# Optimization experiments

Hardware: AMD Instinct MI355X
Metric: run time of the kernel (lower is better)

Reference implementation:

```python
import jax, jax.numpy as jnp
import numpy as np


def setup_inputs() -> dict:
    key = jax.random.key(0)
    ks = jax.random.split(key, 7)
    b, t, c = 2, 2048, 1024
    s = 0.02  # keep pre-softmax logits in a sane range
    return {
        "query": jax.random.normal(ks[0], (b, t, c), jnp.float32),
        "key": jax.random.normal(ks[1], (b, t, c), jnp.float32),
        "value": jax.random.normal(ks[2], (b, t, c), jnp.float32),
        "in_proj_w": jax.random.normal(ks[3], (3 * c, c), jnp.float32) * s,
        "in_proj_b": jax.random.normal(ks[4], (3 * c,), jnp.float32) * s,
        "out_proj_w": jax.random.normal(ks[5], (c, c), jnp.float32) * s,
        "out_proj_b": jax.random.normal(ks[6], (c,), jnp.float32) * s,
        "window_size": 128,
    }


def reference(query, key, value, in_proj_w, in_proj_b, out_proj_w, out_proj_b, window_size):
    num_heads = 16
    b, t, c = query.shape
    hd = c // num_heads
    wq, wk, wv = in_proj_w[:c], in_proj_w[c:2 * c], in_proj_w[2 * c:]
    bq, bk, bv = in_proj_b[:c], in_proj_b[c:2 * c], in_proj_b[2 * c:]
    # project and split heads: [b, h, t, hd]
    q = (query @ wq.T + bq).reshape(b, t, num_heads, hd).transpose(0, 2, 1, 3)
    k = (key @ wk.T + bk).reshape(b, t, num_heads, hd).transpose(0, 2, 1, 3)
    v = (value @ wv.T + bv).reshape(b, t, num_heads, hd).transpose(0, 2, 1, 3)
    # NOTE: torch adds a *float* attn_mask to the logits. The original mask is
    # 1.0 inside the sliding window, 0.0 outside -- an additive +1 bias, NOT -inf.
    idx = jnp.arange(t)
    band = (jnp.abs(idx[:, None] - idx[None, :]) <= window_size).astype(q.dtype)  # [t, t]
    scale = 1.0 / jnp.sqrt(jnp.asarray(hd, q.dtype))
    logits = jnp.einsum("bhqd,bhkd->bhqk", q * scale, k) + band  # [b,h,t,t]
    attn = jax.nn.softmax(logits, axis=-1)
    out = jnp.einsum("bhqk,bhkd->bhqd", attn, v)  # [b,h,t,hd]
    out = out.transpose(0, 2, 1, 3).reshape(b, t, c)
    return out @ out_proj_w.T + out_proj_b
```

## Files before the change

### kernel.cpp

```cpp
#include <hip/hip_runtime.h>

typedef __attribute__((ext_vector_type(8)))  short short8;
typedef __attribute__((ext_vector_type(4)))  float f32x4;
typedef __attribute__((ext_vector_type(16))) float f32x16;

constexpr int B  = 2;
constexpr int T  = 2048;
constexpr int C  = 1024;
constexpr int H  = 16;
constexpr int HD = 64;

__device__ inline unsigned bf16rne(float a){
  unsigned u = __builtin_bit_cast(unsigned, a);
  u += 0x7fffu + ((u >> 16) & 1u);
  return u >> 16;
}
__device__ inline unsigned bf16pair(float a, float b){
  unsigned ua = __builtin_bit_cast(unsigned, a); ua += 0x7fffu + ((ua >> 16) & 1u);
  unsigned ub = __builtin_bit_cast(unsigned, b); ub += 0x7fffu + ((ub >> 16) & 1u);
  return (ua >> 16) | (ub & 0xffff0000u);
}
__device__ inline void gll16(const void* g, void* l){
  __builtin_amdgcn_global_load_lds(
      (const __attribute__((address_space(1))) unsigned*)g,
      (__attribute__((address_space(3))) unsigned*)l, 16, 0, 0);
}
__device__ inline float exp2f_(float x){
#if __has_builtin(__builtin_amdgcn_exp2f)
  return __builtin_amdgcn_exp2f(x);
#else
  return __builtin_exp2f(x);
#endif
}

__global__ void convert_k(const float* __restrict__ ipw, const float* __restrict__ opw,
                          const float* __restrict__ q, const float* __restrict__ k,
                          const float* __restrict__ v, unsigned* __restrict__ dst)
{
  const int i = blockIdx.x * 256 + threadIdx.x;
  const long e = (long)i * 4;
  const float* src; long off;
  if      (e <  3145728) { src = ipw; off = e; }
  else if (e <  4194304) { src = opw; off = e - 3145728; }
  else if (e <  8388608) { src = q;   off = e - 4194304; }
  else if (e < 12582912) { src = k;   off = e - 8388608; }
  else                   { src = v;   off = e - 12582912; }
  const float4 x = *(const float4*)(src + off);
  dst[i*2+0] = bf16pair(x.x, x.y);
  dst[i*2+1] = bf16pair(x.z, x.w);
}

template<int MODE>
__global__ __launch_bounds__(256, 2) void gemm_k(
    const unsigned short* __restrict__ A0, const unsigned short* __restrict__ A1,
    const unsigned short* __restrict__ A2,
    const unsigned short* __restrict__ Wb, const float* __restrict__ bias,
    unsigned short* __restrict__ Qb, unsigned short* __restrict__ Kb,
    unsigned short* __restrict__ Vt, float* __restrict__ outF)
{
  __shared__ __align__(16) char gsm[32768];
  unsigned short* As = (unsigned short*)gsm;
  unsigned short* Bs = (unsigned short*)(gsm + 16384);

  const int tid  = threadIdx.x, lane = tid & 63, wv = tid >> 6;
  const int wm   = wv & 1, wn = wv >> 1;
  const int bn   = blockIdx.x, bm = blockIdx.y;
  const int m16  = lane & 15, quad = lane >> 4;

  const int which = (MODE == 0) ? (bn >> 3) : 0;
  const unsigned short* A = (which == 0) ? A0 : (which == 1 ? A1 : A2);

  f32x4 acc[4][4];
#pragma unroll
  for (int i = 0; i < 4; i++)
#pragma unroll
    for (int j = 0; j < 4; j++) acc[i][j] = (f32x4){0.f, 0.f, 0.f, 0.f};

  const int srow = (lane >> 3);
  const int skp  = (lane & 7) * 8;

  for (int k0 = 0; k0 < 1024; k0 += 64) {
    __syncthreads();
#pragma unroll
    for (int p = 0; p < 4; p++) {
      const int row = wv*32 + p*8 + srow;
      gll16(A  + (size_t)(bm*128 + row)*1024 + k0 + skp, (char*)As + (wv*4+p)*1024);
      gll16(Wb + (size_t)(bn*128 + row)*1024 + k0 + skp, (char*)Bs + (wv*4+p)*1024);
    }
    __syncthreads();

    short8 af[2][4], bf2[2][4];
#pragma unroll
    for (int kh = 0; kh < 2; kh++) {
#pragma unroll
      for (int i = 0; i < 4; i++)
        af[kh][i] = *(const short8*)((const char*)As + (wm*64 + i*16 + m16)*128 + kh*64 + quad*16);
#pragma unroll
      for (int j = 0; j < 4; j++)
        bf2[kh][j] = *(const short8*)((const char*)Bs + (wn*64 + j*16 + m16)*128 + kh*64 + quad*16);
    }
#pragma unroll
    for (int kh = 0; kh < 2; kh++)
#pragma unroll
      for (int i = 0; i < 4; i++)
#pragma unroll
        for (int j = 0; j < 4; j++)
          acc[i][j] = __builtin_amdgcn_mfma_f32_16x16x32_bf16(af[kh][i], bf2[kh][j], acc[i][j], 0,0,0);
  }

  if constexpr (MODE == 1) {
#pragma unroll
    for (int j = 0; j < 4; j++) {
      const int n_e = bn*128 + wn*64 + j*16 + m16;
      const float bj = bias[n_e];
#pragma unroll
      for (int i = 0; i < 4; i++) {
        const int mbase = bm*128 + wm*64 + i*16 + quad*4;
#pragma unroll
        for (int r = 0; r < 4; r++)
          outF[(size_t)(mbase + r) * 1024 + n_e] = acc[i][j][r] + bj;
      }
    }
  } else {
    __syncthreads();
    float* Ls = (float*)gsm;
    const int hbase = (bn & 7) * 2;
    const int b = bm >> 4;
    const int tbase = (bm & 15) * 128;
    if (which < 2) {
      unsigned short* dst = (which == 0 ? Qb : Kb);
#pragma unroll
      for (int j = 0; j < 4; ++j) {
        const float bj = bias[bn*128 + wn*64 + j*16 + m16];
#pragma unroll
        for (int i = 0; i < 4; ++i) {
          const int m0 = wm*64 + i*16 + quad*4;
#pragma unroll
          for (int r = 0; r < 4; ++r)
            Ls[(m0 + r)*36 + wn*16 + m16] = acc[i][j][r] + bj;
        }
        __syncthreads();
#pragma unroll
        for (int r2 = 0; r2 < 2; ++r2) {
          const int v = r2*256 + tid;
          const int m = v & 127, seg = v >> 7;
          const int wn2 = seg >> 1, d0 = j*16 + (seg & 1)*8;
          const float* src = &Ls[m*36 + wn2*16 + (seg & 1)*8];
          const float4 f0 = *(const float4*)src;
          const float4 f1 = *(const float4*)(src + 4);
          uint4 st;
          st.x = bf16pair(f0.x, f0.y); st.y = bf16pair(f0.z, f0.w);
          st.z = bf16pair(f1.x, f1.y); st.w = bf16pair(f1.z, f1.w);
          *(uint4*)&dst[((size_t)((b*16 + hbase + wn2)*2048 + tbase + m))*64 + d0] = st;
        }
        __syncthreads();
      }
    } else {
#pragma unroll
      for (int j = 0; j < 4; ++j) {
        const float bj = bias[bn*128 + wn*64 + j*16 + m16];
        const int col = wn*16 + m16;
#pragma unroll
        for (int i = 0; i < 4; ++i) {
          f32x4 tv = acc[i][j];
          tv[0] += bj; tv[1] += bj; tv[2] += bj; tv[3] += bj;
          *(f32x4*)&Ls[col*132 + wm*64 + i*16 + quad*4] = tv;
        }
        __syncthreads();
#pragma unroll
        for (int r2 = 0; r2 < 2; ++r2) {
          const int v = r2*256 + tid;
          const int n = v >> 4, mseg = v & 15;
          const float* src = &Ls[n*132 + mseg*8];
          const float4 f0 = *(const float4*)src;
          const float4 f1 = *(const float4*)(src + 4);
          uint4 st;
          st.x = bf16pair(f0.x, f0.y); st.y = bf16pair(f0.z, f0.w);
          st.z = bf16pair(f1.x, f1.y); st.w = bf16pair(f1.z, f1.w);
          const int d = j*16 + (n & 15);
          const int hh = hbase + (n >> 4);
          *(uint4*)&Vt[(((size_t)(b*16 + hh))*64 + d)*2048 + tbase + mseg*8] = st;
        }
        __syncthreads();
      }
    }
  }
}

__global__ __launch_bounds__(256, 2) void attn_k(
    const unsigned short* __restrict__ Qb, const unsigned short* __restrict__ Kb,
    const unsigned short* __restrict__ Vt, const int* __restrict__ wptr,
    unsigned short* __restrict__ ctx)
{
  __shared__ __align__(16) char smem[33024];
  float* Om   = (float*)smem;
  float* lbuf = (float*)(smem + 32768);

  const int tid = threadIdx.x, lane = tid & 63, wv = tid >> 6;
  const int wq = wv >> 1, wk = wv & 1;
  const int h = lane >> 5, ln = lane & 31;
  const bool hs = (h == 1);
  const int bh = blockIdx.x, qt = blockIdx.y;
  const int win = *wptr;
  const int q0 = qt * 64 + wq * 32;
  const size_t hb = (size_t)bh * T * HD;

  constexpr float LOG2E = 1.44269504f;
  constexpr float C1    = 0.125f * LOG2E;

  short8 qf[4];
#pragma unroll
  for (int s = 0; s < 4; s++)
    qf[s] = *(const short8*)(Qb + hb + (size_t)(q0 + ln)*64 + s*16 + h*8);

  short8 onesv;
#pragma unroll
  for (int jj = 0; jj < 8; jj++) onesv[jj] = (short)0x3F80;

  f32x16 O0, O1, Lacc, Zv;
#pragma unroll
  for (int r = 0; r < 16; r++) { O0[r] = 0.f; O1[r] = 0.f; Lacc[r] = 0.f; Zv[r] = 0.f; }
  const int tq = q0 + ln;

  const int srow = tid >> 2;
  const int soff = (tid & 3) * 16;
  const int c0   = (tid & 3) * 2;
  const unsigned short* Kg = Kb + hb;
  const unsigned short* Vg = Vt + hb;

  uint4 ka, kb2, va, vb;
  ka  = *(const uint4*)(Kg + (size_t)srow*64 + soff);
  kb2 = *(const uint4*)(Kg + (size_t)srow*64 + soff + 8);
  va  = *(const uint4*)(Vg + (size_t)srow*2048 + soff);
  vb  = *(const uint4*)(Vg + (size_t)srow*2048 + soff + 8);
  {
    char* Kd = smem; char* Vd = smem + 8192;
    *(uint4*)(Kd + c0*1024 + srow*16)     = ka;
    *(uint4*)(Kd + (c0+1)*1024 + srow*16) = kb2;
    *(uint4*)(Vd + c0*1024 + srow*16)     = va;
    *(uint4*)(Vd + (c0+1)*1024 + srow*16) = vb;
  }
  __syncthreads();

  for (int kt = 0; kt < 32; ++kt) {
    if (kt < 31) {
      const int t1 = (kt + 1) * 64;
      ka  = *(const uint4*)(Kg + (size_t)(t1 + srow)*64 + soff);
      kb2 = *(const uint4*)(Kg + (size_t)(t1 + srow)*64 + soff + 8);
      va  = *(const uint4*)(Vg + (size_t)srow*2048 + t1 + soff);
      vb  = *(const uint4*)(Vg + (size_t)srow*2048 + t1 + soff + 8);
    }
    const char* Kl = smem + (kt & 1)*16384;
    const char* Vl = Kl + 8192;

    f32x16 st;
#pragma unroll
    for (int s = 0; s < 4; s++) {
      const short8 kf = *(const short8*)(Kl + (2*s + h)*1024 + (wk*32 + ln)*16);
      st = __builtin_amdgcn_mfma_f32_32x32x16_bf16(kf, qf[s], (s == 0 ? Zv : st), 0, 0, 0);
    }

    const int kb = kt*64 + wk*32;
    int sep = 0;
    if (kb > q0 + 31) sep = kb - (q0 + 31);
    else if (q0 > kb + 31) sep = q0 - (kb + 31);
    const int d1 = kb + 31 - q0, d2 = q0 + 31 - kb;
    const int dmax = max(d1 < 0 ? -d1 : d1, d2 < 0 ? -d2 : d2);

    float pr[16];
    if (sep > win) {
#pragma unroll
      for (int r = 0; r < 16; r++) pr[r] = exp2f_(st[r] * C1);
    } else if (dmax <= win) {
#pragma unroll
      for (int r = 0; r < 16; r++) pr[r] = exp2f_(__builtin_fmaf(st[r], C1, LOG2E));
    } else {
      const int tkb = kb + 4*h;
#pragma unroll
      for (int r = 0; r < 16; r++) {
        const int tk = tkb + (r & 3) + 8*(r >> 2);
        int dd = tq - tk; dd = dd < 0 ? -dd : dd;
        pr[r] = exp2f_(__builtin_fmaf(st[r], C1, dd <= win ? LOG2E : 0.0f));
      }
    }

    unsigned pk[8];
#pragma unroll
    for (int g = 0; g < 8; g++)
      pk[g] = __builtin_amdgcn_perm(__builtin_bit_cast(unsigned, pr[2*g+1]),
                                    __builtin_bit_cast(unsigned, pr[2*g]),
                                    0x07060302u);

#pragma unroll
    for (int c = 0; c < 2; c++) {
      const unsigned sh0 = (unsigned)__shfl_xor((int)pk[4*c+0], 32, 64);
      const unsigned sh1 = (unsigned)__shfl_xor((int)pk[4*c+1], 32, 64);
      const unsigned sh2 = (unsigned)__shfl_xor((int)pk[4*c+2], 32, 64);
      const unsigned sh3 = (unsigned)__shfl_xor((int)pk[4*c+3], 32, 64);
      union { unsigned u[4]; short8 v; } P;
      P.u[0] = hs ? sh2 : pk[4*c+0];
      P.u[1] = hs ? sh3 : pk[4*c+1];
      P.u[2] = hs ? pk[4*c+2] : sh0;
      P.u[3] = hs ? pk[4*c+3] : sh1;
#pragma unroll
      for (int dt = 0; dt < 2; dt++) {
        const short8 vf = *(const short8*)(Vl + (wk*4 + 2*c + h)*1024 + (dt*32 + ln)*16);
        if (dt == 0) O0 = __builtin_amdgcn_mfma_f32_32x32x16_bf16(P.v, vf, O0, 0,0,0);
        else         O1 = __builtin_amdgcn_mfma_f32_32x32x16_bf16(P.v, vf, O1, 0,0,0);
      }
      Lacc = __builtin_amdgcn_mfma_f32_32x32x16_bf16(P.v, onesv, Lacc, 0,0,0);
    }

    if (kt < 31) {
      char* Kd = smem + ((kt + 1) & 1)*16384;
      char* Vd = Kd + 8192;
      *(uint4*)(Kd + c0*1024 + srow*16)     = ka;
      *(uint4*)(Kd + (c0+1)*1024 + srow*16) = kb2;
      *(uint4*)(Vd + c0*1024 + srow*16)     = va;
      *(uint4*)(Vd + (c0+1)*1024 + srow*16) = vb;
      __syncthreads();
    }
  }

  __syncthreads();
  if (wk == 1) {
#pragma unroll
    for (int r = 0; r < 16; r++) {
      Om[wq*2048 + r*64 + lane]        = O0[r];
      Om[wq*2048 + (16 + r)*64 + lane] = O1[r];
    }
    if (ln == 0) {
#pragma unroll
      for (int r = 0; r < 16; r++)
        lbuf[wq*32 + (r & 3) + 8*(r >> 2) + 4*h] = Lacc[r];
    }
  }
  __syncthreads();
  if (wk == 0) {
    const int b = bh >> 4, hh = bh & 15;
#pragma unroll
    for (int r = 0; r < 16; r++) {
      const int qrow = (r & 3) + 8*(r >> 2) + 4*h;
      const float lt = Lacc[r] + lbuf[wq*32 + qrow];
      const float linv = 1.0f / lt;
      const int t = q0 + qrow;
      const float o0 = (O0[r] + Om[wq*2048 + r*64 + lane]) * linv;
      const float o1 = (O1[r] + Om[wq*2048 + (16 + r)*64 + lane]) * linv;
      unsigned short* cp = ctx + (size_t)(b*2048 + t)*1024 + hh*64;
      cp[ln]      = (unsigned short)bf16rne(o0);
      cp[32 + ln] = (unsigned short)bf16rne(o1);
    }
  }
}

extern "C" void kernel_launch(void* const* d_in, const int* in_sizes, int n_in,
                              void* d_out, int out_size, void* d_ws, size_t ws_size,
                              hipStream_t stream)
{
  const float* query = (const float*)d_in[0];
  const float* key   = (const float*)d_in[1];
  const float* value = (const float*)d_in[2];
  const float* ipw   = (const float*)d_in[3];
  const float* ipb   = (const float*)d_in[4];
  const float* opw   = (const float*)d_in[5];
  const float* opb   = (const float*)d_in[6];
  const int*   win   = (const int*)d_in[7];

  char* ws = (char*)d_ws;
  unsigned short* Winbf  = (unsigned short*)(ws);
  unsigned short* Woutbf = (unsigned short*)(ws + 6291456);
  unsigned short* Qin    = (unsigned short*)(ws + 8388608);
  unsigned short* Kin    = (unsigned short*)(ws + 16777216);
  unsigned short* Vin    = (unsigned short*)(ws + 25165824);
  unsigned short* Qb     = (unsigned short*)(ws + 33554432);
  unsigned short* Kb     = (unsigned short*)(ws + 41943040);
  unsigned short* Vt     = (unsigned short*)(ws + 50331648);
  unsigned short* ctx    = (unsigned short*)(ws + 58720256);

  convert_k<<<16384, 256, 0, stream>>>(ipw, opw, query, key, value, (unsigned*)ws);

  gemm_k<0><<<dim3(24, 32), 256, 0, stream>>>(
      Qin, Kin, Vin, Winbf, ipb, Qb, Kb, Vt, nullptr);

  attn_k<<<dim3(32, 32), 256, 0, stream>>>(Qb, Kb, Vt, win, ctx);

  gemm_k<1><<<dim3(8, 32), 256, 0, stream>>>(
      ctx, ctx, ctx, Woutbf, opb, nullptr, nullptr, nullptr, (float*)d_out);
}
```

Before: 245.1 us.

## Store K/V in MFMA-fragment order and load directly into registers, dropping LDS staging

The projection GEMM epilogue now writes K and V in a pre-swizzled layout that matches the MFMA operand fragments of the attention kernel. The attention kernel reads those fragments straight from global memory into registers with a two-tile register double buffer, so it no longer copies K/V tiles through LDS or calls __syncthreads per key tile. LDS use drops to the output reduction buffer only. In exchange, each wave now loads its own K/V fragments, so the two query waves that share a key half fetch the same data twice. The scattered epilogue stores in the GEMM may also coalesce differently, and register pressure goes up.

```diff
diff --git a/kernel.cpp b/kernel.cpp
--- a/kernel.cpp
+++ b/kernel.cpp
@@ -55,8 +55,8 @@
     const unsigned short* __restrict__ A0, const unsigned short* __restrict__ A1,
     const unsigned short* __restrict__ A2,
     const unsigned short* __restrict__ Wb, const float* __restrict__ bias,
-    unsigned short* __restrict__ Qb, unsigned short* __restrict__ Kb,
-    unsigned short* __restrict__ Vt, float* __restrict__ outF)
+    unsigned short* __restrict__ Qb, unsigned short* __restrict__ Kf,
+    unsigned short* __restrict__ Vf, float* __restrict__ outF)
 {
   __shared__ __align__(16) char gsm[32768];
   unsigned short* As = (unsigned short*)gsm;
@@ -128,7 +128,6 @@
     const int b = bm >> 4;
     const int tbase = (bm & 15) * 128;
     if (which < 2) {
-      unsigned short* dst = (which == 0 ? Qb : Kb);
 #pragma unroll
       for (int j = 0; j < 4; ++j) {
         const float bj = bias[bn*128 + wn*64 + j*16 + m16];
@@ -144,14 +143,24 @@
         for (int r2 = 0; r2 < 2; ++r2) {
           const int v = r2*256 + tid;
           const int m = v & 127, seg = v >> 7;
-          const int wn2 = seg >> 1, d0 = j*16 + (seg & 1)*8;
+          const int wn2 = seg >> 1;
           const float* src = &Ls[m*36 + wn2*16 + (seg & 1)*8];
           const float4 f0 = *(const float4*)src;
           const float4 f1 = *(const float4*)(src + 4);
           uint4 st;
           st.x = bf16pair(f0.x, f0.y); st.y = bf16pair(f0.z, f0.w);
           st.z = bf16pair(f1.x, f1.y); st.w = bf16pair(f1.z, f1.w);
-          *(uint4*)&dst[((size_t)((b*16 + hbase + wn2)*2048 + tbase + m))*64 + d0] = st;
+          const int bhh = b*16 + hbase + wn2;
+          if (which == 0) {
+            const int d0 = j*16 + (seg & 1)*8;
+            *(uint4*)&Qb[((size_t)(bhh*2048) + tbase + m)*64 + d0] = st;
+          } else {
+            const int kt = (tbase + m) >> 6;
+            const int wkk = (m >> 5) & 1, ln2 = m & 31;
+            const int h2 = seg & 1;
+            uint4* dp = (uint4*)Kf + ((size_t)(bhh*32 + kt)*8 + j*2 + wkk)*64 + h2*32 + ln2;
+            *dp = st;
+          }
         }
         __syncthreads();
       }
@@ -178,8 +187,13 @@
           st.x = bf16pair(f0.x, f0.y); st.y = bf16pair(f0.z, f0.w);
           st.z = bf16pair(f1.x, f1.y); st.w = bf16pair(f1.z, f1.w);
           const int d = j*16 + (n & 15);
-          const int hh = hbase + (n >> 4);
-          *(uint4*)&Vt[(((size_t)(b*16 + hh))*64 + d)*2048 + tbase + mseg*8] = st;
+          const int bhh = b*16 + hbase + (n >> 4);
+          const int t0 = tbase + mseg*8;
+          const int kt = t0 >> 6, tc = (t0 & 63) >> 3;
+          const int wkk = tc >> 2, cc = (tc >> 1) & 1, h2 = tc & 1;
+          const int dt = d >> 5, ln2 = d & 31;
+          uint4* dp = (uint4*)Vf + (size_t)(bhh*32 + kt)*512 + dt*256 + cc*128 + wkk*64 + h2*32 + ln2;
+          *dp = st;
         }
         __syncthreads();
       }
@@ -188,13 +202,13 @@
 }
 
 __global__ __launch_bounds__(256, 2) void attn_k(
-    const unsigned short* __restrict__ Qb, const unsigned short* __restrict__ Kb,
-    const unsigned short* __restrict__ Vt, const int* __restrict__ wptr,
+    const unsigned short* __restrict__ Qb, const unsigned short* __restrict__ Kf,
+    const unsigned short* __restrict__ Vf, const int* __restrict__ wptr,
     unsigned short* __restrict__ ctx)
 {
-  __shared__ __align__(16) char smem[33024];
+  __shared__ __align__(16) char smem[16896];
   float* Om   = (float*)smem;
-  float* lbuf = (float*)(smem + 32768);
+  float* lbuf = (float*)(smem + 16384);
 
   const int tid = threadIdx.x, lane = tid & 63, wv = tid >> 6;
   const int wq = wv >> 1, wk = wv & 1;
@@ -222,42 +236,21 @@
   for (int r = 0; r < 16; r++) { O0[r] = 0.f; O1[r] = 0.f; Lacc[r] = 0.f; Zv[r] = 0.f; }
   const int tq = q0 + ln;
 
-  const int srow = tid >> 2;
-  const int soff = (tid & 3) * 16;
-  const int c0   = (tid & 3) * 2;
-  const unsigned short* Kg = Kb + hb;
-  const unsigned short* Vg = Vt + hb;
-
-  uint4 ka, kb2, va, vb;
-  ka  = *(const uint4*)(Kg + (size_t)srow*64 + soff);
-  kb2 = *(const uint4*)(Kg + (size_t)srow*64 + soff + 8);
-  va  = *(const uint4*)(Vg + (size_t)srow*2048 + soff);
-  vb  = *(const uint4*)(Vg + (size_t)srow*2048 + soff + 8);
-  {
-    char* Kd = smem; char* Vd = smem + 8192;
-    *(uint4*)(Kd + c0*1024 + srow*16)     = ka;
-    *(uint4*)(Kd + (c0+1)*1024 + srow*16) = kb2;
-    *(uint4*)(Vd + c0*1024 + srow*16)     = va;
-    *(uint4*)(Vd + (c0+1)*1024 + srow*16) = vb;
-  }
-  __syncthreads();
-
-  for (int kt = 0; kt < 32; ++kt) {
-    if (kt < 31) {
-      const int t1 = (kt + 1) * 64;
-      ka  = *(const uint4*)(Kg + (size_t)(t1 + srow)*64 + soff);
-      kb2 = *(const uint4*)(Kg + (size_t)(t1 + srow)*64 + soff + 8);
-      va  = *(const uint4*)(Vg + (size_t)srow*2048 + t1 + soff);
-      vb  = *(const uint4*)(Vg + (size_t)srow*2048 + t1 + soff + 8);
-    }
-    const char* Kl = smem + (kt & 1)*16384;
-    const char* Vl = Kl + 8192;
-
+  const uint4* kbase = (const uint4*)Kf + (size_t)bh*32*512 + wk*64 + lane;
+  const uint4* vbase = (const uint4*)Vf + (size_t)bh*32*512 + wk*64 + lane;
+
+  uint4 kA[4], vA[4], kB[4], vB[4];
+#pragma unroll
+  for (int s = 0; s < 4; s++) kA[s] = kbase[s*128];
+#pragma unroll
+  for (int u = 0; u < 4; u++) vA[u] = vbase[(u >> 1)*256 + (u & 1)*128];
+
+  auto body = [&](int kt, uint4 (&ka)[4], uint4 (&va)[4]) {
     f32x16 st;
 #pragma unroll
     for (int s = 0; s < 4; s++) {
-      const short8 kf = *(const short8*)(Kl + (2*s + h)*1024 + (wk*32 + ln)*16);
-      st = __builtin_amdgcn_mfma_f32_32x32x16_bf16(kf, qf[s], (s == 0 ? Zv : st), 0, 0, 0);
+      const short8 kf2 = __builtin_bit_cast(short8, ka[s]);
+      st = __builtin_amdgcn_mfma_f32_32x32x16_bf16(kf2, qf[s], (s == 0 ? Zv : st), 0, 0, 0);
     }
 
     const int kb = kt*64 + wk*32;
@@ -304,22 +297,31 @@
       P.u[3] = hs ? pk[4*c+3] : sh1;
 #pragma unroll
       for (int dt = 0; dt < 2; dt++) {
-        const short8 vf = *(const short8*)(Vl + (wk*4 + 2*c + h)*1024 + (dt*32 + ln)*16);
-        if (dt == 0) O0 = __builtin_amdgcn_mfma_f32_32x32x16_bf16(P.v, vf, O0, 0,0,0);
-        else         O1 = __builtin_amdgcn_mfma_f32_32x32x16_bf16(P.v, vf, O1, 0,0,0);
+        const short8 vf2 = __builtin_bit_cast(short8, va[dt*2 + c]);
+        if (dt == 0) O0 = __builtin_amdgcn_mfma_f32_32x32x16_bf16(P.v, vf2, O0, 0,0,0);
+        else         O1 = __builtin_amdgcn_mfma_f32_32x32x16_bf16(P.v, vf2, O1, 0,0,0);
       }
       Lacc = __builtin_amdgcn_mfma_f32_32x32x16_bf16(P.v, onesv, Lacc, 0,0,0);
     }
-
-    if (kt < 31) {
-      char* Kd = smem + ((kt + 1) & 1)*16384;
-      char* Vd = Kd + 8192;
-      *(uint4*)(Kd + c0*1024 + srow*16)     = ka;
-      *(uint4*)(Kd + (c0+1)*1024 + srow*16) = kb2;
-      *(uint4*)(Vd + c0*1024 + srow*16)     = va;
-      *(uint4*)(Vd + (c0+1)*1024 + srow*16) = vb;
-      __syncthreads();
-    }
+  };
+
+  for (int kt = 0; kt < 32; kt += 2) {
+    {
+      const size_t o = (size_t)(kt + 1) * 512;
+#pragma unroll
+      for (int s = 0; s < 4; s++) kB[s] = kbase[o + s*128];
+#pragma unroll
+      for (int u = 0; u < 4; u++) vB[u] = vbase[o + (u >> 1)*256 + (u & 1)*128];
+    }
+    body(kt, kA, vA);
+    if (kt + 2 < 32) {
+      const size_t o = (size_t)(kt + 2) * 512;
+#pragma unroll
+      for (int s = 0; s < 4; s++) kA[s] = kbase[o + s*128];
+#pragma unroll
+      for (int u = 0; u < 4; u++) vA[u] = vbase[o + (u >> 1)*256 + (u & 1)*128];
+    }
+    body(kt + 1, kB, vB);
   }
 
   __syncthreads();
@@ -373,16 +375,16 @@
   unsigned short* Kin    = (unsigned short*)(ws + 16777216);
   unsigned short* Vin    = (unsigned short*)(ws + 25165824);
   unsigned short* Qb     = (unsigned short*)(ws + 33554432);
-  unsigned short* Kb     = (unsigned short*)(ws + 41943040);
-  unsigned short* Vt     = (unsigned short*)(ws + 50331648);
+  unsigned short* Kf     = (unsigned short*)(ws + 41943040);
+  unsigned short* Vf     = (unsigned short*)(ws + 50331648);
   unsigned short* ctx    = (unsigned short*)(ws + 58720256);
 
   convert_k<<<16384, 256, 0, stream>>>(ipw, opw, query, key, value, (unsigned*)ws);
 
   gemm_k<0><<<dim3(24, 32), 256, 0, stream>>>(
-      Qin, Kin, Vin, Winbf, ipb, Qb, Kb, Vt, nullptr);
-
-  attn_k<<<dim3(32, 32), 256, 0, stream>>>(Qb, Kb, Vt, win, ctx);
+      Qin, Kin, Vin, Winbf, ipb, Qb, Kf, Vf, nullptr);
+
+  attn_k<<<dim3(32, 32), 256, 0, stream>>>(Qb, Kf, Vf, win, ctx);
 
   gemm_k<1><<<dim3(8, 32), 256, 0, stream>>>(
       ctx, ctx, ctx, Woutbf, opb, nullptr, nullptr, nullptr, (float*)d_out);
```

Result: faster. 229.8 us (-6.2%).
